# Kernel optimization log

Hardware: AMD Instinct MI355X
Metric: run time of the kernel (lower is better)

Reference implementation:

```python
import jax, jax.numpy as jnp
import numpy as np

N_NODES = 20000
N_EDGES = 640000
CHANNELS = 128
EDGE_ATTR_DIM = 1


def setup_inputs() -> dict:
    key = jax.random.key(0)
    ks = jax.random.split(key, 10)
    C, E, N = CHANNELS, N_EDGES, N_NODES
    x_a = jax.random.normal(ks[0], (N, C), dtype=jnp.float32)
    edge_index = jax.random.randint(ks[1], (2, E), 0, N, dtype=jnp.int64)
    edge_attr = jax.random.uniform(ks[2], (E, EDGE_ATTR_DIM), dtype=jnp.float32)
    # Linear params (stored as [in, out]); scaled like torch default init
    g_in = 2 * C + EDGE_ATTR_DIM
    g_w = jax.random.uniform(ks[3], (g_in, C), jnp.float32, -1, 1) / np.sqrt(g_in)
    g_b = jax.random.uniform(ks[4], (C,), jnp.float32, -1, 1) / np.sqrt(g_in)
    f_w = jax.random.uniform(ks[5], (2 * C, C), jnp.float32, -1, 1) / np.sqrt(2 * C)
    f_b = jax.random.uniform(ks[6], (C,), jnp.float32, -1, 1) / np.sqrt(2 * C)
    cls_w = jax.random.uniform(ks[7], (C, 1), jnp.float32, -1, 1) / np.sqrt(C)
    cls_b = jax.random.uniform(ks[8], (1,), jnp.float32, -1, 1) / np.sqrt(C)
    return {"x_a": x_a, "edge_index": edge_index, "edge_attr": edge_attr,
            "g_w": g_w, "g_b": g_b, "f_w": f_w, "f_b": f_b,
            "cls_w": cls_w, "cls_b": cls_b}


def reference(x_a, edge_index, edge_attr, g_w, g_b, f_w, f_b, cls_w, cls_b):
    # PyG MessagePassing (flow source_to_target): x_j = x[src], x_i = x[dst]
    src = edge_index[0]
    dst = edge_index[1]
    N = x_a.shape[0]
    # message: g([x_i, x_j, e_ij])  -> [E, C]
    z_ij = jnp.concatenate([x_a[dst], x_a[src], edge_attr], axis=-1)
    msg = z_ij @ g_w + g_b
    # aggregate: scatter-mean over destination nodes (empty nodes -> 0)
    sums = jax.ops.segment_sum(msg, dst, num_segments=N)
    cnt = jax.ops.segment_sum(jnp.ones((dst.shape[0], 1), x_a.dtype), dst,
                              num_segments=N)
    aggr = sums / jnp.maximum(cnt, 1.0)
    # update: f([x, aggr])
    h = jnp.concatenate([x_a, aggr], axis=-1) @ f_w + f_b
    # classifier + sigmoid + threshold
    probs = jax.nn.sigmoid(h @ cls_w + cls_b)
    y = probs > 0.5
    return (y, probs)
```

## Files before the change

kernel.cpp:

```cpp
#include <hip/hip_runtime.h>
#include <math.h>

#define NNODES 20000
#define NEDGES 640000
#define C 128

#define NB1 256
#define BT 1024

#define NCHUNK 128
#define EPC (NEDGES / NCHUNK)
#define HALFN (NNODES / 2)

#define CNT_SHIFT 26
#define EDGE_BIAS (1 << 19)
#define SUM_MASK 0x03FFFFFFu

__global__ void __launch_bounds__(BT)
k_node(const float* __restrict__ x,
       const float* __restrict__ g_w, const float* __restrict__ g_b,
       const float* __restrict__ f_w, const float* __restrict__ f_b,
       const float* __restrict__ cls_w, const float* __restrict__ cls_b,
       float* __restrict__ xu, float* __restrict__ xp,
       float* __restrict__ r, float* __restrict__ scal)
{
    __shared__ float csh[C], vsh[C], ush[C], psh[C], qsh[C];
    const int tid = threadIdx.x;
    const int pair = tid >> 2;
    const int prt  = tid & 3;
    const int k = pair & 127;
    const int h = pair >> 7;

    if (tid < C) csh[tid] = cls_w[tid];
    __syncthreads();

    const float4* fw4 = (const float4*)f_w;
    const float4* gw4 = (const float4*)g_w;
    const float4* cs4 = (const float4*)csh;

    {
        const float4* row = fw4 + (size_t)(h * C + k) * (C / 4) + prt * 8;
        const float4* cc  = cs4 + prt * 8;
        float s = 0.f;
        #pragma unroll
        for (int j = 0; j < 8; ++j) {
            float4 a = row[j], c = cc[j];
            s += a.x * c.x + a.y * c.y + a.z * c.z + a.w * c.w;
        }
        s += __shfl_down(s, 2);
        s += __shfl_down(s, 1);
        if (prt == 0) { if (h == 0) ush[k] = s; else vsh[k] = s; }
    }
    __syncthreads();

    const float4* vs4 = (const float4*)vsh;
    {
        const float4* row = gw4 + (size_t)(h * C + k) * (C / 4) + prt * 8;
        const float4* vv  = vs4 + prt * 8;
        float s = 0.f;
        #pragma unroll
        for (int j = 0; j < 8; ++j) {
            float4 a = row[j], c = vv[j];
            s += a.x * c.x + a.y * c.y + a.z * c.z + a.w * c.w;
        }
        s += __shfl_down(s, 2);
        s += __shfl_down(s, 1);
        if (prt == 0) { if (h == 0) psh[k] = s; else qsh[k] = s; }
    }
    __syncthreads();

    if (blockIdx.x == 0 && tid < 192) {
        int w = tid >> 6, lane = tid & 63;
        float a, b;
        if (w == 0)      { a = g_b[lane] * vsh[lane];          b = g_b[lane + 64] * vsh[lane + 64]; }
        else if (w == 1) { a = g_w[256 * C + lane] * vsh[lane]; b = g_w[256 * C + lane + 64] * vsh[lane + 64]; }
        else             { a = f_b[lane] * csh[lane];          b = f_b[lane + 64] * csh[lane + 64]; }
        float s = a + b;
        for (int off = 32; off > 0; off >>= 1) s += __shfl_down(s, off);
        if (lane == 0) scal[w] = (w == 2) ? s + cls_b[0] : s;
    }

    {
        int w = tid >> 6, lane = tid & 63;
        int gwave = blockIdx.x * (BT / 64) + w;
        float2 uu = ((const float2*)ush)[lane];
        float2 pp = ((const float2*)psh)[lane];
        float2 qq = ((const float2*)qsh)[lane];

        for (int n = gwave; n < NNODES; n += NB1 * (BT / 64)) {
            float2 xx = ((const float2*)(x + (size_t)n * C))[lane];
            float du = xx.x * uu.x + xx.y * uu.y;
            float dp = xx.x * pp.x + xx.y * pp.y;
            float dq = xx.x * qq.x + xx.y * qq.y;
            for (int off = 32; off > 0; off >>= 1) {
                du += __shfl_down(du, off);
                dp += __shfl_down(dp, off);
                dq += __shfl_down(dq, off);
            }
            if (lane == 0) { xu[n] = du; xp[n] = dp; r[n] = dq; }
        }
    }
}

__global__ void __launch_bounds__(BT)
k_edge(const int* __restrict__ ei, const float* __restrict__ attr,
       const float* __restrict__ r, const float* __restrict__ scal,
       unsigned int* __restrict__ part)
{
    __shared__ unsigned int lacc[HALFN];
    const int tid = threadIdx.x;
    const int chunk = blockIdx.x & (NCHUNK - 1);
    const int h     = blockIdx.x >> 7;
    const int nbase = h * HALFN;

    uint4* l4 = (uint4*)lacc;
    for (int i = tid; i < HALFN / 4; i += BT) l4[i] = make_uint4(0u, 0u, 0u, 0u);
    __syncthreads();

    const float gev = scal[1];
    const int ebase = chunk * EPC;
    for (int i = tid; i < EPC; i += BT) {
        int e = ebase + i;
        int s = ei[e];
        int d = ei[NEDGES + e];
        unsigned int idx = (unsigned int)(d - nbase);
        if (idx < HALFN) {
            float t = r[s] + attr[e] * gev;
            int fix = __float2int_rn(t * 65536.0f);
            atomicAdd(&lacc[idx], (1u << CNT_SHIFT) + (unsigned int)(fix + EDGE_BIAS));
        }
    }
    __syncthreads();

    uint4* mp4 = (uint4*)(part + (size_t)(chunk * 2 + h) * HALFN);
    for (int i = tid; i < HALFN / 4; i += BT) mp4[i] = l4[i];
}

__global__ void __launch_bounds__(256)
k_final(const float* __restrict__ xu, const float* __restrict__ xp,
        const unsigned int* __restrict__ part,
        const float* __restrict__ scal, float* __restrict__ out)
{
    int t = threadIdx.x;
    int quad = t >> 2;
    int prt  = t & 3;
    int n = blockIdx.x * 64 + quad;

    int sumfix = 0, cnt = 0;
    if (n < NNODES) {
        int h   = (n >= HALFN) ? 1 : 0;
        int idx = n - h * HALFN;
        const unsigned int* pb = part + (size_t)((prt * 32) * 2 + h) * HALFN + idx;
        #pragma unroll
        for (int b = 0; b < NCHUNK / 4; ++b) {
            unsigned int v = pb[(size_t)b * 2 * HALFN];
            int c = (int)(v >> CNT_SHIFT);
            cnt += c;
            sumfix += (int)(v & SUM_MASK) - (c << 19);
        }
    }
    sumfix += __shfl_down(sumfix, 1);
    sumfix += __shfl_down(sumfix, 2);
    cnt    += __shfl_down(cnt, 1);
    cnt    += __shfl_down(cnt, 2);

    if (prt == 0 && n < NNODES) {
        float sacc = (float)sumfix * (1.0f / 65536.0f);
        float cmax = fmaxf((float)cnt, 1.0f);
        float cfac = (cnt > 0) ? 1.0f : 0.0f;
        float logit = xu[n] + cfac * (xp[n] + scal[0]) + sacc / cmax + scal[2];
        float pr = 1.0f / (1.0f + expf(-logit));
        out[n] = (pr > 0.5f) ? 1.0f : 0.0f;
        out[NNODES + n] = pr;
    }
}

extern "C" void kernel_launch(void* const* d_in, const int* in_sizes, int n_in,
                              void* d_out, int out_size, void* d_ws, size_t ws_size,
                              hipStream_t stream) {
    const float* x_a       = (const float*)d_in[0];
    const int*   ei        = (const int*)d_in[1];
    const float* edge_attr = (const float*)d_in[2];
    const float* g_w       = (const float*)d_in[3];
    const float* g_b       = (const float*)d_in[4];
    const float* f_w       = (const float*)d_in[5];
    const float* f_b       = (const float*)d_in[6];
    const float* cls_w     = (const float*)d_in[7];
    const float* cls_b     = (const float*)d_in[8];
    float* out = (float*)d_out;

    unsigned int* part = (unsigned int*)d_ws;
    float* xu   = (float*)d_ws + (size_t)NCHUNK * NNODES;
    float* xp   = xu + NNODES;
    float* r    = xp + NNODES;
    float* scal = r + NNODES;

    k_node<<<NB1, BT, 0, stream>>>(x_a, g_w, g_b, f_w, f_b, cls_w, cls_b,
                                   xu, xp, r, scal);

    k_edge<<<NCHUNK * 2, BT, 0, stream>>>(ei, edge_attr, r, scal, part);

    k_final<<<(NNODES + 63) / 64, 256, 0, stream>>>(xu, xp, part, scal, out);
}
```

Baseline: 102.2 us.

## Cache node scalars in LDS and split edge accumulation into node quarters

```diff
diff --git a/kernel.cpp b/kernel.cpp
--- a/kernel.cpp
+++ b/kernel.cpp
@@ -8,9 +8,10 @@
 #define NB1 256
 #define BT 1024
 
-#define NCHUNK 128
+#define NCHUNK 64
 #define EPC (NEDGES / NCHUNK)
-#define HALFN (NNODES / 2)
+#define QSPLIT 4
+#define QN (NNODES / QSPLIT)
 
 #define CNT_SHIFT 26
 #define EDGE_BIAS (1 << 19)
@@ -107,14 +108,18 @@
        const float* __restrict__ r, const float* __restrict__ scal,
        unsigned int* __restrict__ part)
 {
-    __shared__ unsigned int lacc[HALFN];
+    __shared__ float rsh[NNODES];
+    __shared__ unsigned int lacc[QN];
     const int tid = threadIdx.x;
     const int chunk = blockIdx.x & (NCHUNK - 1);
-    const int h     = blockIdx.x >> 7;
-    const int nbase = h * HALFN;
-
+    const int q     = blockIdx.x >> 6;
+    const int nbase = q * QN;
+
+    float4* rs4 = (float4*)rsh;
+    const float4* r4 = (const float4*)r;
+    for (int i = tid; i < NNODES / 4; i += BT) rs4[i] = r4[i];
     uint4* l4 = (uint4*)lacc;
-    for (int i = tid; i < HALFN / 4; i += BT) l4[i] = make_uint4(0u, 0u, 0u, 0u);
+    for (int i = tid; i < QN / 4; i += BT) l4[i] = make_uint4(0u, 0u, 0u, 0u);
     __syncthreads();
 
     const float gev = scal[1];
@@ -124,16 +129,16 @@
         int s = ei[e];
         int d = ei[NEDGES + e];
         unsigned int idx = (unsigned int)(d - nbase);
-        if (idx < HALFN) {
-            float t = r[s] + attr[e] * gev;
+        if (idx < QN) {
+            float t = rsh[s] + attr[e] * gev;
             int fix = __float2int_rn(t * 65536.0f);
             atomicAdd(&lacc[idx], (1u << CNT_SHIFT) + (unsigned int)(fix + EDGE_BIAS));
         }
     }
     __syncthreads();
 
-    uint4* mp4 = (uint4*)(part + (size_t)(chunk * 2 + h) * HALFN);
-    for (int i = tid; i < HALFN / 4; i += BT) mp4[i] = l4[i];
+    uint4* mp4 = (uint4*)(part + (size_t)(chunk * QSPLIT + q) * QN);
+    for (int i = tid; i < QN / 4; i += BT) mp4[i] = l4[i];
 }
 
 __global__ void __launch_bounds__(256)
@@ -148,12 +153,12 @@
 
     int sumfix = 0, cnt = 0;
     if (n < NNODES) {
-        int h   = (n >= HALFN) ? 1 : 0;
-        int idx = n - h * HALFN;
-        const unsigned int* pb = part + (size_t)((prt * 32) * 2 + h) * HALFN + idx;
+        int q   = n / QN;
+        int idx = n - q * QN;
+        const unsigned int* pb = part + (size_t)((prt * (NCHUNK / 4)) * QSPLIT + q) * QN + idx;
         #pragma unroll
         for (int b = 0; b < NCHUNK / 4; ++b) {
-            unsigned int v = pb[(size_t)b * 2 * HALFN];
+            unsigned int v = pb[(size_t)b * QSPLIT * QN];
             int c = (int)(v >> CNT_SHIFT);
             cnt += c;
             sumfix += (int)(v & SUM_MASK) - (c << 19);
@@ -198,7 +203,7 @@
     k_node<<<NB1, BT, 0, stream>>>(x_a, g_w, g_b, f_w, f_b, cls_w, cls_b,
                                    xu, xp, r, scal);
 
-    k_edge<<<NCHUNK * 2, BT, 0, stream>>>(ei, edge_attr, r, scal, part);
+    k_edge<<<NCHUNK * QSPLIT, BT, 0, stream>>>(ei, edge_attr, r, scal, part);
 
     k_final<<<(NNODES + 63) / 64, 256, 0, stream>>>(xu, xp, part, scal, out);
 }
```

Result: no change. 102.9 us (+0.7%).

## Split edge scatter into eight node ranges, halve chunks, vectorize edge loads

Applied to the files above, without the earlier changes.

```diff
diff --git a/kernel.cpp b/kernel.cpp
--- a/kernel.cpp
+++ b/kernel.cpp
@@ -8,9 +8,10 @@
 #define NB1 256
 #define BT 1024
 
-#define NCHUNK 128
+#define NCHUNK 64
 #define EPC (NEDGES / NCHUNK)
-#define HALFN (NNODES / 2)
+#define ESPLIT 8
+#define TN (NNODES / ESPLIT)
 
 #define CNT_SHIFT 26
 #define EDGE_BIAS (1 << 19)
@@ -107,33 +108,54 @@
        const float* __restrict__ r, const float* __restrict__ scal,
        unsigned int* __restrict__ part)
 {
-    __shared__ unsigned int lacc[HALFN];
+    __shared__ unsigned int lacc[TN];
     const int tid = threadIdx.x;
     const int chunk = blockIdx.x & (NCHUNK - 1);
-    const int h     = blockIdx.x >> 7;
-    const int nbase = h * HALFN;
+    const int oct   = blockIdx.x >> 6;
+    const int nbase = oct * TN;
 
     uint4* l4 = (uint4*)lacc;
-    for (int i = tid; i < HALFN / 4; i += BT) l4[i] = make_uint4(0u, 0u, 0u, 0u);
+    for (int i = tid; i < TN / 4; i += BT) l4[i] = make_uint4(0u, 0u, 0u, 0u);
     __syncthreads();
 
     const float gev = scal[1];
     const int ebase = chunk * EPC;
-    for (int i = tid; i < EPC; i += BT) {
-        int e = ebase + i;
-        int s = ei[e];
-        int d = ei[NEDGES + e];
-        unsigned int idx = (unsigned int)(d - nbase);
-        if (idx < HALFN) {
-            float t = r[s] + attr[e] * gev;
-            int fix = __float2int_rn(t * 65536.0f);
-            atomicAdd(&lacc[idx], (1u << CNT_SHIFT) + (unsigned int)(fix + EDGE_BIAS));
-        }
-    }
-    __syncthreads();
-
-    uint4* mp4 = (uint4*)(part + (size_t)(chunk * 2 + h) * HALFN);
-    for (int i = tid; i < HALFN / 4; i += BT) mp4[i] = l4[i];
+    for (int g = tid; g < EPC / 4; g += BT) {
+        int e = ebase + g * 4;
+        int4   s4 = *(const int4*)(ei + e);
+        int4   d4 = *(const int4*)(ei + NEDGES + e);
+        float4 a4 = *(const float4*)(attr + e);
+
+        unsigned int i0 = (unsigned int)(d4.x - nbase);
+        unsigned int i1 = (unsigned int)(d4.y - nbase);
+        unsigned int i2 = (unsigned int)(d4.z - nbase);
+        unsigned int i3 = (unsigned int)(d4.w - nbase);
+
+        if (i0 < TN) {
+            float t = r[s4.x] + a4.x * gev;
+            int fix = __float2int_rn(t * 65536.0f);
+            atomicAdd(&lacc[i0], (1u << CNT_SHIFT) + (unsigned int)(fix + EDGE_BIAS));
+        }
+        if (i1 < TN) {
+            float t = r[s4.y] + a4.y * gev;
+            int fix = __float2int_rn(t * 65536.0f);
+            atomicAdd(&lacc[i1], (1u << CNT_SHIFT) + (unsigned int)(fix + EDGE_BIAS));
+        }
+        if (i2 < TN) {
+            float t = r[s4.z] + a4.z * gev;
+            int fix = __float2int_rn(t * 65536.0f);
+            atomicAdd(&lacc[i2], (1u << CNT_SHIFT) + (unsigned int)(fix + EDGE_BIAS));
+        }
+        if (i3 < TN) {
+            float t = r[s4.w] + a4.w * gev;
+            int fix = __float2int_rn(t * 65536.0f);
+            atomicAdd(&lacc[i3], (1u << CNT_SHIFT) + (unsigned int)(fix + EDGE_BIAS));
+        }
+    }
+    __syncthreads();
+
+    uint4* mp4 = (uint4*)(part + (size_t)(chunk * ESPLIT + oct) * TN);
+    for (int i = tid; i < TN / 4; i += BT) mp4[i] = l4[i];
 }
 
 __global__ void __launch_bounds__(256)
@@ -148,12 +170,12 @@
 
     int sumfix = 0, cnt = 0;
     if (n < NNODES) {
-        int h   = (n >= HALFN) ? 1 : 0;
-        int idx = n - h * HALFN;
-        const unsigned int* pb = part + (size_t)((prt * 32) * 2 + h) * HALFN + idx;
+        int oct = n / TN;
+        int idx = n - oct * TN;
+        const unsigned int* pb = part + (size_t)((prt * (NCHUNK / 4)) * ESPLIT + oct) * TN + idx;
         #pragma unroll
         for (int b = 0; b < NCHUNK / 4; ++b) {
-            unsigned int v = pb[(size_t)b * 2 * HALFN];
+            unsigned int v = pb[(size_t)b * ESPLIT * TN];
             int c = (int)(v >> CNT_SHIFT);
             cnt += c;
             sumfix += (int)(v & SUM_MASK) - (c << 19);
@@ -198,7 +220,7 @@
     k_node<<<NB1, BT, 0, stream>>>(x_a, g_w, g_b, f_w, f_b, cls_w, cls_b,
                                    xu, xp, r, scal);
 
-    k_edge<<<NCHUNK * 2, BT, 0, stream>>>(ei, edge_attr, r, scal, part);
+    k_edge<<<NCHUNK * ESPLIT, BT, 0, stream>>>(ei, edge_attr, r, scal, part);
 
     k_final<<<(NNODES + 63) / 64, 256, 0, stream>>>(xu, xp, part, scal, out);
 }
```

After: 99.87 us. 2.3% less time.
